# Optimization experiments

Measured on AMD Instinct MI355X. Metric: run time of the kernel, lower is better.

## Reference

```python
import jax, jax.numpy as jnp
import numpy as np

EPS = 1e-6  # torch F.cosine_similarity eps


def setup_inputs() -> dict:
    key = jax.random.key(0)
    k1, = jax.random.split(key, 1)
    N, M, D = 1024, 10, 768
    dvecs = jax.random.normal(k1, (N, M, D), dtype=jnp.float32)
    w = jnp.full((1,), 10.0, dtype=jnp.float32)   # init_w
    b = jnp.full((1,), -5.0, dtype=jnp.float32)   # init_b
    return {"dvecs": dvecs, "w": w, "b": b}


def _ge2e_softmax_loss(dvecs, w, b):
    N, M, D = dvecs.shape
    sums = jnp.sum(dvecs, axis=1)                      # (N, D)
    ctrds = sums / M                                   # full centroids
    excl = (sums[:, None, :] - dvecs) / (M - 1)        # (N, M, D) leave-one-out centroids

    dnorm = jnp.maximum(jnp.linalg.norm(dvecs, axis=-1), EPS)   # (N, M)
    cnorm = jnp.maximum(jnp.linalg.norm(ctrds, axis=-1), EPS)   # (N,)
    enorm = jnp.maximum(jnp.linalg.norm(excl, axis=-1), EPS)    # (N, M)

    # cosine sim of every utterance to every full centroid: (N, M, N)
    sim_all = jnp.einsum('nmd,kd->nmk', dvecs, ctrds) / (dnorm[:, :, None] * cnorm[None, None, :])
    # cosine sim of each utterance to its own excluded centroid: (N, M)
    sim_own = jnp.sum(dvecs * excl, axis=-1) / (dnorm * enorm)

    own_mask = jnp.eye(N, dtype=bool)[:, None, :]      # (N, 1, N)
    sim = jnp.where(own_mask, sim_own[:, :, None], sim_all)

    sim = sim * w[0] + b[0]
    losses = -jax.nn.log_softmax(sim, axis=2)          # (N, M, N)
    # pick entry [s, u, s] for each utterance
    own = jnp.take_along_axis(losses, jnp.broadcast_to(jnp.arange(N)[:, None, None], (N, M, 1)), axis=2)
    return jnp.sum(own)


def reference(dvecs, w, b):
    return _ge2e_softmax_loss(dvecs, w, b)
```

## Files before the change

### kernel.cpp

```cpp
#include <hip/hip_runtime.h>
#include <hip/hip_bf16.h>

#define EPS 1e-6f

typedef __attribute__((ext_vector_type(4))) float f32x4;

__device__ inline unsigned int pack_fp8x4(float x, float y, float z, float w) {
  int r = 0;
  r = __builtin_amdgcn_cvt_pk_fp8_f32(x, y, r, false);
  r = __builtin_amdgcn_cvt_pk_fp8_f32(z, w, r, true);
  return (unsigned int)r;
}

__global__ void __launch_bounds__(192) ge2e_pre(
    const float* __restrict__ dv, unsigned int* __restrict__ a8u,
    unsigned int* __restrict__ c8u, float* __restrict__ simown,
    float* __restrict__ rowsum, float* __restrict__ out) {
  const int n = blockIdx.x, t = threadIdx.x;
  if (n == 0 && t == 0) out[0] = 0.f;
  const float* base = dv + (size_t)n * 7680;
  float4 v[10];
  float4 s4 = make_float4(0.f, 0.f, 0.f, 0.f);
#pragma unroll
  for (int m = 0; m < 10; ++m) {
    v[m] = *reinterpret_cast<const float4*>(&base[m * 768 + 4 * t]);
    s4.x += v[m].x; s4.y += v[m].y; s4.z += v[m].z; s4.w += v[m].w;
  }
  float part[21];
#pragma unroll
  for (int m = 0; m < 10; ++m) {
    part[m]      = v[m].x * s4.x + v[m].y * s4.y + v[m].z * s4.z + v[m].w * s4.w;
    part[10 + m] = v[m].x * v[m].x + v[m].y * v[m].y + v[m].z * v[m].z + v[m].w * v[m].w;
  }
  part[20] = s4.x * s4.x + s4.y * s4.y + s4.z * s4.z + s4.w * s4.w;
#pragma unroll
  for (int k = 0; k < 21; ++k) {
#pragma unroll
    for (int off = 32; off >= 1; off >>= 1) part[k] += __shfl_xor(part[k], off);
  }
  __shared__ float red[3][21];
  __shared__ float bc[21];
  const int lane = t & 63, wid = t >> 6;
  if (lane == 0) {
#pragma unroll
    for (int k = 0; k < 21; ++k) red[wid][k] = part[k];
  }
  __syncthreads();
  if (t < 21) bc[t] = red[0][t] + red[1][t] + red[2][t];
  __syncthreads();
  const float ss = bc[20];
  const float rc = 1.0f / fmaxf(sqrtf(ss), 10.0f * EPS);
  c8u[n * 192 + t] = pack_fp8x4(s4.x * rc, s4.y * rc, s4.z * rc, s4.w * rc);
#pragma unroll
  for (int m = 0; m < 10; ++m) {
    float rd = 1.0f / fmaxf(sqrtf(bc[10 + m]), EPS);
    a8u[(size_t)(n * 10 + m) * 192 + t] =
        pack_fp8x4(v[m].x * rd, v[m].y * rd, v[m].z * rd, v[m].w * rd);
  }
  if (t < 10) {
    float dot = bc[t], sq = bc[10 + t];
    float dn = fmaxf(sqrtf(sq), EPS);
    float en = fmaxf(sqrtf(fmaxf(ss - 2.f * dot + sq, 0.f)) * (1.0f / 9.0f), EPS);
    simown[n * 10 + t] = ((dot - sq) * (1.0f / 9.0f)) / (dn * en);
    rowsum[n * 10 + t] = 0.f;
  }
}

__global__ void __launch_bounds__(512, 4) ge2e_gemm(
    const unsigned char* __restrict__ a8, const unsigned char* __restrict__ c8,
    const float* __restrict__ simown, const float* __restrict__ wp,
    float* __restrict__ rowsum) {
  __shared__ __align__(16) unsigned char As[2][20480];
  __shared__ __align__(16) unsigned char Bs[2][4096];
  const int t = threadIdx.x;
  const int lane = t & 63, wid = t >> 6;
  const int bx = blockIdx.x;
  const int wg = (bx & 7) * 64 + (bx >> 3);
  const int rb = wg >> 4, cb = wg & 15;
  const int row0 = rb * 320, col0 = cb * 64;
  const int wm = wid >> 1, wn = wid & 1;
  const int l15 = lane & 15, lg = lane >> 4;
  const int srow = lane >> 2;
  const int sk = (lane & 3) ^ ((lane >> 3) & 3);

  f32x4 acc[5][2];
#pragma unroll
  for (int i = 0; i < 5; ++i)
#pragma unroll
    for (int j = 0; j < 2; ++j) acc[i][j] = (f32x4){0.f, 0.f, 0.f, 0.f};

  auto STAGE = [&](int buf, int ks) {
#pragma unroll
    for (int j = 0; j < 3; ++j) {
      const int g = wid * 3 + j;
      if (g < 20) {
        const unsigned char* src =
            a8 + (size_t)(row0 + g * 16 + srow) * 768 + ks * 64 + sk * 16;
        __builtin_amdgcn_global_load_lds(
            (const __attribute__((address_space(1))) unsigned int*)src,
            (__attribute__((address_space(3))) unsigned int*)&As[buf][g * 1024],
            16, 0, 0);
      } else {
        const unsigned char* src =
            c8 + (size_t)(col0 + (g - 20) * 16 + srow) * 768 + ks * 64 + sk * 16;
        __builtin_amdgcn_global_load_lds(
            (const __attribute__((address_space(1))) unsigned int*)src,
            (__attribute__((address_space(3))) unsigned int*)&Bs[buf][(g - 20) * 1024],
            16, 0, 0);
      }
    }
  };

  auto ldA = [&](int buf, int kh, int fr) -> long long {
    const int row = wm * 80 + fr * 16 + l15;
    const int slot = (kh * 2 + (lg >> 1)) ^ ((row >> 1) & 3);
    return *(const long long*)&As[buf][row * 64 + slot * 16 + (lg & 1) * 8];
  };
  auto ldB = [&](int buf, int kh, int fc) -> long long {
    const int row = wn * 32 + fc * 16 + l15;
    const int slot = (kh * 2 + (lg >> 1)) ^ ((row >> 1) & 3);
    return *(const long long*)&Bs[buf][row * 64 + slot * 16 + (lg & 1) * 8];
  };

  auto COMPUTE = [&](int buf) {
    long long af[5][2], bf[2][2];
#pragma unroll
    for (int fc = 0; fc < 2; ++fc)
#pragma unroll
      for (int kh = 0; kh < 2; ++kh) bf[fc][kh] = ldB(buf, kh, fc);
#pragma unroll
    for (int fr = 0; fr < 5; ++fr)
#pragma unroll
      for (int kh = 0; kh < 2; ++kh) af[fr][kh] = ldA(buf, kh, fr);
    __builtin_amdgcn_s_setprio(1);
#pragma unroll
    for (int kh = 0; kh < 2; ++kh)
#pragma unroll
      for (int fr = 0; fr < 5; ++fr)
#pragma unroll
        for (int fc = 0; fc < 2; ++fc)
          acc[fr][fc] = __builtin_amdgcn_mfma_f32_16x16x32_fp8_fp8(
              af[fr][kh], bf[fc][kh], acc[fr][fc], 0, 0, 0);
    __builtin_amdgcn_s_setprio(0);
  };

  STAGE(0, 0);
#pragma unroll
  for (int s = 0; s < 12; ++s) {
    if (s < 11) {
      STAGE((s + 1) & 1, s + 1);
      asm volatile("s_waitcnt vmcnt(3)" ::: "memory");
    } else {
      asm volatile("s_waitcnt vmcnt(0)" ::: "memory");
    }
    __builtin_amdgcn_s_barrier();
    COMPUTE(s & 1);
    if (s < 11) __builtin_amdgcn_s_barrier();
  }

  const float wv = wp[0];
  const int R0 = row0 + wm * 80, C0 = col0 + wn * 32;
#pragma unroll
  for (int fr = 0; fr < 5; ++fr) {
#pragma unroll
    for (int r = 0; r < 4; ++r) {
      const int grow = R0 + fr * 16 + lg * 4 + r;
      const int ownc = grow / 10;
      float sm = 0.f;
#pragma unroll
      for (int fc = 0; fc < 2; ++fc) {
        const int gcol = C0 + fc * 16 + l15;
        float vv = wv * acc[fr][fc][r];
        if (gcol == ownc) vv = wv * simown[grow];
        sm += __expf(vv);
      }
#pragma unroll
      for (int off = 1; off < 16; off <<= 1) sm += __shfl_xor(sm, off, 16);
      if (l15 == 0) atomicAdd(&rowsum[grow], sm);
    }
  }
}

__global__ void __launch_bounds__(256) ge2e_final(
    const float* __restrict__ rowsum, const float* __restrict__ simown,
    const float* __restrict__ wp, float* __restrict__ out) {
  const int i = blockIdx.x * 256 + threadIdx.x;
  const float wv = wp[0];
  float loss = logf(rowsum[i]) - wv * simown[i];
#pragma unroll
  for (int off = 32; off >= 1; off >>= 1) loss += __shfl_xor(loss, off);
  __shared__ float red[4];
  const int lane = threadIdx.x & 63, wid = threadIdx.x >> 6;
  if (lane == 0) red[wid] = loss;
  __syncthreads();
  if (threadIdx.x == 0) atomicAdd(out, red[0] + red[1] + red[2] + red[3]);
}

extern "C" void kernel_launch(void* const* d_in, const int* in_sizes, int n_in,
                              void* d_out, int out_size, void* d_ws, size_t ws_size,
                              hipStream_t stream) {
  (void)in_sizes; (void)n_in; (void)out_size; (void)ws_size;
  const float* dv = (const float*)d_in[0];
  const float* wp = (const float*)d_in[1];

  unsigned char* a8 = (unsigned char*)d_ws;
  unsigned char* c8 = (unsigned char*)d_ws + 7864320;
  float* simown = (float*)((char*)d_ws + 8650752);
  float* rowsum = (float*)((char*)d_ws + 8691712);
  float* out = (float*)d_out;

  ge2e_pre<<<1024, 192, 0, stream>>>(dv, (unsigned int*)a8, (unsigned int*)c8,
                                     simown, rowsum, out);
  ge2e_gemm<<<512, 512, 0, stream>>>(a8, c8, simown, wp, rowsum);
  ge2e_final<<<40, 256, 0, stream>>>(rowsum, simown, wp, out);
}
```

Before: 43.59 us.

## Keep centroid tile in registers and stream A in full-K row slabs

The GEMM is restructured so each block loads its 128-column centroid slice once into registers (full K=768), then streams 32-row slabs of utterance vectors with full K through double-buffered LDS. Each slab's exp-sums are accumulated in shared memory, with a single global atomic per row at the end. The own-centroid replacement moves to the final kernel, which subtracts exp of the diagonal GEMM value and adds exp of simown. The changes aim to cut redundant B loads, per-k-step barriers and global atomics, at the cost of higher register pressure (48 long longs for B), fewer blocks (256) and lower occupancy.

```diff
diff --git a/kernel.cpp b/kernel.cpp
--- a/kernel.cpp
+++ b/kernel.cpp
@@ -66,127 +66,139 @@
   }
 }
 
-__global__ void __launch_bounds__(512, 4) ge2e_gemm(
+__global__ void __launch_bounds__(512, 2) ge2e_gemm(
     const unsigned char* __restrict__ a8, const unsigned char* __restrict__ c8,
-    const float* __restrict__ simown, const float* __restrict__ wp,
-    float* __restrict__ rowsum) {
-  __shared__ __align__(16) unsigned char As[2][20480];
-  __shared__ __align__(16) unsigned char Bs[2][4096];
+    const float* __restrict__ wp, float* __restrict__ rowsum,
+    float* __restrict__ diag) {
+  __shared__ __align__(16) unsigned char As[49152];
+  __shared__ float rowAcc[320];
   const int t = threadIdx.x;
   const int lane = t & 63, wid = t >> 6;
   const int bx = blockIdx.x;
-  const int wg = (bx & 7) * 64 + (bx >> 3);
-  const int rb = wg >> 4, cb = wg & 15;
-  const int row0 = rb * 320, col0 = cb * 64;
-  const int wm = wid >> 1, wn = wid & 1;
+  const int wg = (bx & 7) * 32 + (bx >> 3);
+  const int rp = wg >> 3, cb = wg & 7;
+  const int rowPart = rp * 320, col0 = cb * 128;
+  const int wm = wid >> 2, wn = wid & 3;
   const int l15 = lane & 15, lg = lane >> 4;
-  const int srow = lane >> 2;
-  const int sk = (lane & 3) ^ ((lane >> 3) & 3);
-
-  f32x4 acc[5][2];
-#pragma unroll
-  for (int i = 0; i < 5; ++i)
-#pragma unroll
-    for (int j = 0; j < 2; ++j) acc[i][j] = (f32x4){0.f, 0.f, 0.f, 0.f};
-
-  auto STAGE = [&](int buf, int ks) {
+  const float wv = wp[0];
+
+  if (t < 320) rowAcc[t] = 0.f;
+
+  long long bReg[2][24];
+#pragma unroll
+  for (int h = 0; h < 2; ++h) {
+#pragma unroll
+    for (int j = 0; j < 6; ++j) {
+      const int cidx = (wid * 6 + j) * 64 + lane;
+      const int col = cidx / 48, slot = cidx - col * 48;
+      const int srcSlot = slot ^ (col & 7);
+      const unsigned char* src =
+          c8 + (size_t)(col0 + h * 64 + col) * 768 + srcSlot * 16;
+      __builtin_amdgcn_global_load_lds(
+          (const __attribute__((address_space(1))) unsigned int*)src,
+          (__attribute__((address_space(3))) unsigned int*)&As[(wid * 6 + j) * 1024],
+          16, 0, 0);
+    }
+    asm volatile("s_waitcnt vmcnt(0)" ::: "memory");
+    __syncthreads();
+    if ((wn >> 1) == h) {
+#pragma unroll
+      for (int cs = 0; cs < 2; ++cs) {
+        const int row = (wn & 1) * 32 + cs * 16 + l15;
+#pragma unroll
+        for (int kk = 0; kk < 24; ++kk) {
+          const int slotK = 2 * kk + (lg >> 1);
+          bReg[cs][kk] = *(const long long*)
+              &As[row * 768 + ((slotK ^ (row & 7)) << 4) + (lg & 1) * 8];
+        }
+      }
+    }
+    __syncthreads();
+  }
+
+  auto STAGE_A = [&](int buf, int s) {
 #pragma unroll
     for (int j = 0; j < 3; ++j) {
-      const int g = wid * 3 + j;
-      if (g < 20) {
-        const unsigned char* src =
-            a8 + (size_t)(row0 + g * 16 + srow) * 768 + ks * 64 + sk * 16;
-        __builtin_amdgcn_global_load_lds(
-            (const __attribute__((address_space(1))) unsigned int*)src,
-            (__attribute__((address_space(3))) unsigned int*)&As[buf][g * 1024],
-            16, 0, 0);
-      } else {
-        const unsigned char* src =
-            c8 + (size_t)(col0 + (g - 20) * 16 + srow) * 768 + ks * 64 + sk * 16;
-        __builtin_amdgcn_global_load_lds(
-            (const __attribute__((address_space(1))) unsigned int*)src,
-            (__attribute__((address_space(3))) unsigned int*)&Bs[buf][(g - 20) * 1024],
-            16, 0, 0);
-      }
+      const int cidx = (wid * 3 + j) * 64 + lane;
+      const int row = cidx / 48, slot = cidx - row * 48;
+      const int srcSlot = slot ^ (row & 7);
+      const unsigned char* src =
+          a8 + (size_t)(rowPart + s * 32 + row) * 768 + srcSlot * 16;
+      __builtin_amdgcn_global_load_lds(
+          (const __attribute__((address_space(1))) unsigned int*)src,
+          (__attribute__((address_space(3))) unsigned int*)
+              &As[buf * 24576 + (wid * 3 + j) * 1024],
+          16, 0, 0);
     }
   };
 
-  auto ldA = [&](int buf, int kh, int fr) -> long long {
-    const int row = wm * 80 + fr * 16 + l15;
-    const int slot = (kh * 2 + (lg >> 1)) ^ ((row >> 1) & 3);
-    return *(const long long*)&As[buf][row * 64 + slot * 16 + (lg & 1) * 8];
-  };
-  auto ldB = [&](int buf, int kh, int fc) -> long long {
-    const int row = wn * 32 + fc * 16 + l15;
-    const int slot = (kh * 2 + (lg >> 1)) ^ ((row >> 1) & 3);
-    return *(const long long*)&Bs[buf][row * 64 + slot * 16 + (lg & 1) * 8];
-  };
-
-  auto COMPUTE = [&](int buf) {
-    long long af[5][2], bf[2][2];
-#pragma unroll
-    for (int fc = 0; fc < 2; ++fc)
-#pragma unroll
-      for (int kh = 0; kh < 2; ++kh) bf[fc][kh] = ldB(buf, kh, fc);
-#pragma unroll
-    for (int fr = 0; fr < 5; ++fr)
-#pragma unroll
-      for (int kh = 0; kh < 2; ++kh) af[fr][kh] = ldA(buf, kh, fr);
-    __builtin_amdgcn_s_setprio(1);
-#pragma unroll
-    for (int kh = 0; kh < 2; ++kh)
-#pragma unroll
-      for (int fr = 0; fr < 5; ++fr)
-#pragma unroll
-        for (int fc = 0; fc < 2; ++fc)
-          acc[fr][fc] = __builtin_amdgcn_mfma_f32_16x16x32_fp8_fp8(
-              af[fr][kh], bf[fc][kh], acc[fr][fc], 0, 0, 0);
-    __builtin_amdgcn_s_setprio(0);
-  };
-
-  STAGE(0, 0);
-#pragma unroll
-  for (int s = 0; s < 12; ++s) {
-    if (s < 11) {
-      STAGE((s + 1) & 1, s + 1);
+  const int aRow = wm * 16 + l15;
+  const int aOff0 = aRow * 768 + (lg & 1) * 8;
+  const int ar7 = aRow & 7, ac0 = lg >> 1;
+
+  STAGE_A(0, 0);
+  for (int s = 0; s < 10; ++s) {
+    const int buf = s & 1;
+    if (s < 9) {
+      STAGE_A(buf ^ 1, s + 1);
       asm volatile("s_waitcnt vmcnt(3)" ::: "memory");
     } else {
       asm volatile("s_waitcnt vmcnt(0)" ::: "memory");
     }
     __builtin_amdgcn_s_barrier();
-    COMPUTE(s & 1);
-    if (s < 11) __builtin_amdgcn_s_barrier();
-  }
-
-  const float wv = wp[0];
-  const int R0 = row0 + wm * 80, C0 = col0 + wn * 32;
-#pragma unroll
-  for (int fr = 0; fr < 5; ++fr) {
+
+    f32x4 acc[2][2];
+#pragma unroll
+    for (int fc = 0; fc < 2; ++fc)
+#pragma unroll
+      for (int p = 0; p < 2; ++p) acc[fc][p] = (f32x4){0.f, 0.f, 0.f, 0.f};
+
+    __builtin_amdgcn_s_setprio(1);
+#pragma unroll
+    for (int kk = 0; kk < 24; ++kk) {
+      const int slotK = 2 * kk + ac0;
+      const long long a = *(const long long*)
+          &As[buf * 24576 + aOff0 + ((slotK ^ ar7) << 4)];
+      acc[0][kk & 1] = __builtin_amdgcn_mfma_f32_16x16x32_fp8_fp8(
+          a, bReg[0][kk], acc[0][kk & 1], 0, 0, 0);
+      acc[1][kk & 1] = __builtin_amdgcn_mfma_f32_16x16x32_fp8_fp8(
+          a, bReg[1][kk], acc[1][kk & 1], 0, 0, 0);
+    }
+    __builtin_amdgcn_s_setprio(0);
+
 #pragma unroll
     for (int r = 0; r < 4; ++r) {
-      const int grow = R0 + fr * 16 + lg * 4 + r;
+      const int lrow = s * 32 + wm * 16 + lg * 4 + r;
+      const int grow = rowPart + lrow;
       const int ownc = grow / 10;
       float sm = 0.f;
 #pragma unroll
       for (int fc = 0; fc < 2; ++fc) {
-        const int gcol = C0 + fc * 16 + l15;
-        float vv = wv * acc[fr][fc][r];
-        if (gcol == ownc) vv = wv * simown[grow];
-        sm += __expf(vv);
+        const int gcol = col0 + wn * 32 + fc * 16 + l15;
+        const float vv = acc[fc][0][r] + acc[fc][1][r];
+        if (gcol == ownc) diag[grow] = vv;
+        sm += __expf(wv * vv);
       }
 #pragma unroll
       for (int off = 1; off < 16; off <<= 1) sm += __shfl_xor(sm, off, 16);
-      if (l15 == 0) atomicAdd(&rowsum[grow], sm);
-    }
-  }
+      if (l15 == 0) atomicAdd(&rowAcc[lrow], sm);
+    }
+    __builtin_amdgcn_s_barrier();
+  }
+
+  __syncthreads();
+  if (t < 320) atomicAdd(&rowsum[rowPart + t], rowAcc[t]);
 }
 
 __global__ void __launch_bounds__(256) ge2e_final(
     const float* __restrict__ rowsum, const float* __restrict__ simown,
-    const float* __restrict__ wp, float* __restrict__ out) {
+    const float* __restrict__ diag, const float* __restrict__ wp,
+    float* __restrict__ out) {
   const int i = blockIdx.x * 256 + threadIdx.x;
   const float wv = wp[0];
-  float loss = logf(rowsum[i]) - wv * simown[i];
+  const float so = simown[i];
+  const float corrected = rowsum[i] - __expf(wv * diag[i]) + __expf(wv * so);
+  float loss = logf(corrected) - wv * so;
 #pragma unroll
   for (int off = 32; off >= 1; off >>= 1) loss += __shfl_xor(loss, off);
   __shared__ float red[4];
@@ -207,10 +219,11 @@
   unsigned char* c8 = (unsigned char*)d_ws + 7864320;
   float* simown = (float*)((char*)d_ws + 8650752);
   float* rowsum = (float*)((char*)d_ws + 8691712);
+  float* diag   = (float*)((char*)d_ws + 8732672);
   float* out = (float*)d_out;
 
   ge2e_pre<<<1024, 192, 0, stream>>>(dv, (unsigned int*)a8, (unsigned int*)c8,
                                      simown, rowsum, out);
-  ge2e_gemm<<<512, 512, 0, stream>>>(a8, c8, simown, wp, rowsum);
-  ge2e_final<<<40, 256, 0, stream>>>(rowsum, simown, wp, out);
-}
+  ge2e_gemm<<<256, 512, 0, stream>>>(a8, c8, wp, rowsum, diag);
+  ge2e_final<<<40, 256, 0, stream>>>(rowsum, simown, diag, wp, out);
+}
```

Measured after the change: 44.91 us. 1.03x slower.
